# Optimization experiments

Measured on AMD Instinct MI355X. Metric: run time of the kernel, lower is better.

## Reference

```python
import jax, jax.numpy as jnp
import numpy as np

B, T, D, K = 16, 4096, 256, 1024

def setup_inputs() -> dict:
    key = jax.random.key(0)
    k1, k2 = jax.random.split(key)
    inputs = jax.random.normal(k1, (B, T, D), dtype=jnp.float32)
    codebook = jax.random.normal(k2, (K, D), dtype=jnp.float32)
    return {"inputs": inputs, "codebook": codebook}

def reference(inputs, codebook):
    # argmin over squared distance == argmin over L2 distance (cdist p=2).
    x2 = jnp.sum(inputs * inputs, axis=-1, keepdims=True)          # [B,T,1]
    c2 = jnp.sum(codebook * codebook, axis=-1)                      # [K]
    xc = jnp.einsum('btd,kd->btk', inputs, codebook)                # [B,T,K]
    d2 = x2 + c2[None, None, :] - 2.0 * xc                          # [B,T,K]
    assignment = jnp.argmin(d2, axis=-1)                            # [B,T]
    quantized = codebook[assignment]                                # [B,T,D]
    # Straight-through estimator
    out = jax.lax.stop_gradient(quantized - inputs) + inputs
    return out
```

## Files before the change

kernel.cpp:

```cpp
#include <hip/hip_runtime.h>
#include <float.h>


typedef _Float16 f16;
typedef f16 f16x8 __attribute__((ext_vector_type(8)));
typedef f16 f16x4 __attribute__((ext_vector_type(4)));
typedef float f32x4 __attribute__((ext_vector_type(4)));

#define DDIM    256
#define KCODES  1024
#define NTOK    65536
#define TOKB    64
#define SMARGIN 0.1f

__global__ __launch_bounds__(256) void vq_prep(const float* __restrict__ cb,
                                               f16* __restrict__ cht,
                                               float* __restrict__ c2,
                                               unsigned* __restrict__ count) {
    const int k    = blockIdx.x * 4 + (threadIdx.x >> 6);
    const int lane = threadIdx.x & 63;
    const float4 v = *(const float4*)(cb + (size_t)k * DDIM + 4 * lane);
    f16x4 h; h[0] = (f16)v.x; h[1] = (f16)v.y; h[2] = (f16)v.z; h[3] = (f16)v.w;
    const int ct = k >> 4, m = k & 15;
    const int e  = 4 * lane;
    const int kt = e >> 5;
    const int s  = (e & 31) >> 3;
    const int j0 = e & 7;
    const int L  = s * 16 + m;
    *(f16x4*)(cht + ((size_t)(ct * 8 + kt) * 64 + L) * 8 + j0) = h;
    float ssum = v.x * v.x + v.y * v.y + v.z * v.z + v.w * v.w;
    #pragma unroll
    for (int off = 32; off > 0; off >>= 1) ssum += __shfl_down(ssum, off, 64);
    if (lane == 0) c2[k] = ssum;
    if (blockIdx.x == 0 && threadIdx.x == 0) *count = 0u;
}

#define SLICE(CUR, S, NPTR, NS) do {                                                \
    _Pragma("unroll")                                                               \
    for (int ci = 0; ci < 4; ++ci)                                                  \
        _Pragma("unroll")                                                           \
        for (int ti = 0; ti < 2; ++ti)                                              \
            acc[ci][ti] = __builtin_amdgcn_mfma_f32_16x16x32_f16(                   \
                CUR[ci], bfrag[ti][S], acc[ci][ti], 0, 0, 0);                       \
    _Pragma("unroll")                                                               \
    for (int ci = 0; ci < 4; ++ci)                                                  \
        CUR[ci] = *(const f16x8*)((NPTR) + ci * 4096 + (NS) * 512);                 \
} while (0)

__global__ __launch_bounds__(256, 3) void vq_main(const float* __restrict__ xg,
                                                  const f16* __restrict__ cht,
                                                  const float* __restrict__ c2,
                                                  const float* __restrict__ cb,
                                                  float* __restrict__ out,
                                                  unsigned* __restrict__ count,
                                                  unsigned* __restrict__ list) {
    __shared__ float c2s[KCODES];
    __shared__ float wmv[2][TOKB];
    __shared__ int   wmi[2][TOKB];
    __shared__ float wms[2][TOKB];
    __shared__ int   idx_s[TOKB];

    const int t    = threadIdx.x;
    const int wave = t >> 6, lane = t & 63;
    const int wm   = wave >> 1;
    const int tn   = wave & 1;
    const int q    = lane >> 4;
    const int m16  = lane & 15;
    const int tok0 = blockIdx.x * TOKB;

    *(float4*)&c2s[t * 4] = *(const float4*)(c2 + t * 4);
    __syncthreads();

    const f16* aw = cht + wm * 16384 + lane * 8;

    f16x8 afA[4], afB[4];
    #pragma unroll
    for (int ci = 0; ci < 4; ++ci) afA[ci] = *(const f16x8*)(aw + ci * 4096 + 0 * 512);
    #pragma unroll
    for (int ci = 0; ci < 4; ++ci) afB[ci] = *(const f16x8*)(aw + ci * 4096 + 1 * 512);

    f16x8 bfrag[2][8];
    #pragma unroll
    for (int ti = 0; ti < 2; ++ti) {
        const size_t row = (size_t)(tok0 + tn * 32 + ti * 16 + m16) * DDIM;
        #pragma unroll
        for (int ks = 0; ks < 8; ++ks) {
            const float* p = xg + row + ks * 32 + q * 8;
            const float4 u0 = *(const float4*)(p);
            const float4 u1 = *(const float4*)(p + 4);
            f16x8 b;
            b[0] = (f16)u0.x; b[1] = (f16)u0.y; b[2] = (f16)u0.z; b[3] = (f16)u0.w;
            b[4] = (f16)u1.x; b[5] = (f16)u1.y; b[6] = (f16)u1.z; b[7] = (f16)u1.w;
            bfrag[ti][ks] = b;
        }
    }

    float rb1[2], rb2[2];
    #pragma unroll
    for (int ti = 0; ti < 2; ++ti) { rb1[ti] = -FLT_MAX; rb2[ti] = -FLT_MAX; }

    #pragma unroll 1
    for (int nc = 0; nc < 8; ++nc) {
        f32x4 acc[4][2];
        #pragma unroll
        for (int ci = 0; ci < 4; ++ci) {
            f32x4 cv = *(const f32x4*)&c2s[nc * 128 + wm * 64 + ci * 16 + q * 4];
            cv = cv * -0.5f;
            #pragma unroll
            for (int ti = 0; ti < 2; ++ti) acc[ci][ti] = cv;
        }

        const f16* an = aw + nc * 32768;
        const f16* ax = aw + ((nc + 1) & 7) * 32768;

        __builtin_amdgcn_s_setprio(1);
        SLICE(afA, 0, an, 2);
        SLICE(afB, 1, an, 3);
        SLICE(afA, 2, an, 4);
        SLICE(afB, 3, an, 5);
        SLICE(afA, 4, an, 6);
        SLICE(afB, 5, an, 7);
        SLICE(afA, 6, ax, 0);
        SLICE(afB, 7, ax, 1);
        __builtin_amdgcn_s_setprio(0);

        #pragma unroll
        for (int ti = 0; ti < 2; ++ti) {
            #pragma unroll
            for (int ci = 0; ci < 4; ++ci) {
                #pragma unroll
                for (int r = 0; r < 4; ++r) {
                    const unsigned pv = (__float_as_uint(acc[ci][ti][r]) & ~127u)
                                        | (unsigned)(127 - (nc * 16 + ci * 4 + r));
                    const float pf = __uint_as_float(pv);
                    rb2[ti] = fmaxf(rb2[ti], fminf(rb1[ti], pf));
                    rb1[ti] = fmaxf(rb1[ti], pf);
                }
            }
        }
    }

    #pragma unroll
    for (int ti = 0; ti < 2; ++ti) {
        const int jj = 127 - (int)(__float_as_uint(rb1[ti]) & 127u);
        int   i1 = (jj >> 4) * 128 + wm * 64 + ((jj >> 2) & 3) * 16 + q * 4 + (jj & 3);
        float b1 = rb1[ti], b2 = rb2[ti];
        #pragma unroll
        for (int sft = 0; sft < 2; ++sft) {
            const int off = 16 << sft;
            const float ob1 = __shfl_xor(b1, off, 64);
            const float ob2 = __shfl_xor(b2, off, 64);
            const int   oi1 = __shfl_xor(i1, off, 64);
            const bool better = (ob1 > b1) || (ob1 == b1 && oi1 < i1);
            b2 = fmaxf(fmaxf(b2, ob2), fminf(b1, ob1));
            b1 = better ? ob1 : b1;
            i1 = better ? oi1 : i1;
        }
        if (lane < 16) {
            const int tl = tn * 32 + ti * 16 + m16;
            wmv[wm][tl] = b1; wmi[wm][tl] = i1; wms[wm][tl] = b2;
        }
    }
    __syncthreads();

    if (t < TOKB) {
        const float a1 = wmv[0][t], a2 = wms[0][t];
        const int   ai = wmi[0][t];
        const float b1_ = wmv[1][t], b2_ = wms[1][t];
        const int   bi_ = wmi[1][t];
        const bool bb = (b1_ > a1) || (b1_ == a1 && bi_ < ai);
        const float c1 = bb ? b1_ : a1;
        const int   ci_ = bb ? bi_ : ai;
        const float cs = fmaxf(fmaxf(a2, b2_), fminf(a1, b1_));
        idx_s[t] = ci_;
        if (c1 - cs < SMARGIN) {
            const unsigned p = atomicAdd(count, 1u);
            list[p] = tok0 + t;
        }
    }
    __syncthreads();

    #pragma unroll
    for (int i = 0; i < 16; ++i) {
        const int f   = i * 256 + t;
        const int tok = f >> 6, d4 = f & 63;
        const int code = idx_s[tok];
        const float4 v = *(const float4*)(cb + (size_t)code * DDIM + 4 * d4);
        *(float4*)(out + (size_t)(tok0 + tok) * DDIM + 4 * d4) = v;
    }
}

__global__ __launch_bounds__(256) void vq_rescue(const float* __restrict__ xg,
                                                 const float* __restrict__ cb,
                                                 const float* __restrict__ c2,
                                                 const unsigned* __restrict__ count,
                                                 const unsigned* __restrict__ list,
                                                 float* __restrict__ out) {
    __shared__ float xls[8][DDIM];
    __shared__ float rv[4][8];
    __shared__ int   ri[4][8];
    __shared__ int   bidx[8];

    const int t = threadIdx.x;
    const int wave = t >> 6, lane = t & 63;
    const unsigned n = *count;

    for (unsigned base = blockIdx.x * 8; base < n; base += gridDim.x * 8) {
        const int nb = (int)min(8u, n - base);
        __syncthreads();
        #pragma unroll
        for (int i = 0; i < 2; ++i) {
            const int f = t + 256 * i;
            const int row = f >> 6, d4 = f & 63;
            if (row < nb)
                *(float4*)&xls[row][4 * d4] =
                    *(const float4*)(xg + (size_t)list[base + row] * DDIM + 4 * d4);
        }
        __syncthreads();

        float acc[4][8];
        #pragma unroll
        for (int j = 0; j < 4; ++j)
            #pragma unroll
            for (int tk = 0; tk < 8; ++tk) acc[j][tk] = 0.0f;

        for (int d4 = 0; d4 < 64; ++d4) {
            float4 cv[4];
            #pragma unroll
            for (int j = 0; j < 4; ++j)
                cv[j] = *(const float4*)(cb + (size_t)(4 * t + j) * DDIM + 4 * d4);
            #pragma unroll
            for (int tk = 0; tk < 8; ++tk) {
                const float4 xv = *(const float4*)&xls[tk][4 * d4];
                #pragma unroll
                for (int j = 0; j < 4; ++j) {
                    float a = acc[j][tk];
                    a = fmaf(cv[j].x, xv.x, a);
                    a = fmaf(cv[j].y, xv.y, a);
                    a = fmaf(cv[j].z, xv.z, a);
                    a = fmaf(cv[j].w, xv.w, a);
                    acc[j][tk] = a;
                }
            }
        }

        #pragma unroll
        for (int tk = 0; tk < 8; ++tk) {
            if (tk < nb) {
                float b1 = FLT_MAX; int i1 = 0;
                #pragma unroll
                for (int j = 0; j < 4; ++j) {
                    const float d = fmaf(-2.0f, acc[j][tk], c2[4 * t + j]);
                    if (d < b1) { b1 = d; i1 = 4 * t + j; }
                }
                #pragma unroll
                for (int off = 32; off > 0; off >>= 1) {
                    const float ov = __shfl_xor(b1, off, 64);
                    const int   oi = __shfl_xor(i1, off, 64);
                    if (ov < b1 || (ov == b1 && oi < i1)) { b1 = ov; i1 = oi; }
                }
                if (lane == 0) { rv[wave][tk] = b1; ri[wave][tk] = i1; }
            }
        }
        __syncthreads();
        if (t < 8 && t < nb) {
            float bv = rv[0][t]; int bi = ri[0][t];
            #pragma unroll
            for (int w = 1; w < 4; ++w)
                if (rv[w][t] < bv || (rv[w][t] == bv && ri[w][t] < bi)) {
                    bv = rv[w][t]; bi = ri[w][t];
                }
            bidx[t] = bi;
        }
        __syncthreads();

        #pragma unroll
        for (int i = 0; i < 2; ++i) {
            const int f = t + 256 * i;
            const int row = f >> 6, d4 = f & 63;
            if (row < nb) {
                const int code = bidx[row];
                const float4 v = *(const float4*)(cb + (size_t)code * DDIM + 4 * d4);
                *(float4*)(out + (size_t)list[base + row] * DDIM + 4 * d4) = v;
            }
        }
    }
}

extern "C" void kernel_launch(void* const* d_in, const int* in_sizes, int n_in,
                              void* d_out, int out_size, void* d_ws, size_t ws_size,
                              hipStream_t stream) {
    const float* x  = (const float*)d_in[0];
    const float* cb = (const float*)d_in[1];
    float* out = (float*)d_out;

    char* ws = (char*)d_ws;
    f16*      cht   = (f16*)ws;
    float*    c2    = (float*)(ws + 524288);
    unsigned* count = (unsigned*)(ws + 528448);
    unsigned* list  = (unsigned*)(ws + 528512);

    hipLaunchKernelGGL(vq_prep,   dim3(KCODES / 4), dim3(256), 0, stream, cb, cht, c2, count);
    hipLaunchKernelGGL(vq_main,   dim3(NTOK / TOKB), dim3(256), 0, stream,
                       x, cht, c2, cb, out, count, list);
    hipLaunchKernelGGL(vq_rescue, dim3(1024),       dim3(256), 0, stream,
                       x, cb, c2, count, list, out);
}
```

Before: 240.7 us.

## Stage token tile in LDS and split codebook across all four waves

Each block now converts its 64-token input tile to f16 once, stores it in shared memory in MFMA layout, and every wave covers all 64 tokens. Work is split over waves by codebook slice (4 x 64 codes per chunk) instead of a 2x2 token/code split. Each codebook fragment loaded from global memory now feeds 4 token tiles instead of 2, halving codebook traffic per token. In exchange B fragments are reloaded from LDS every slice, LDS use grows by 32KB, and the accumulator register footprint doubles, which may hurt occupancy at the 3-blocks-per-CU bound.

Result: slower. 282.4 us (+17.3%).

```diff
diff --git a/kernel.cpp b/kernel.cpp
--- a/kernel.cpp
+++ b/kernel.cpp
@@ -35,16 +35,19 @@
     if (blockIdx.x == 0 && threadIdx.x == 0) *count = 0u;
 }
 
-#define SLICE(CUR, S, NPTR, NS) do {                                                \
+#define SLICE(AF, BF, S, NAP, NBS) do {                                             \
     _Pragma("unroll")                                                               \
     for (int ci = 0; ci < 4; ++ci)                                                  \
         _Pragma("unroll")                                                           \
-        for (int ti = 0; ti < 2; ++ti)                                              \
+        for (int ti = 0; ti < 4; ++ti)                                              \
             acc[ci][ti] = __builtin_amdgcn_mfma_f32_16x16x32_f16(                   \
-                CUR[ci], bfrag[ti][S], acc[ci][ti], 0, 0, 0);                       \
+                AF[ci], BF[ti], acc[ci][ti], 0, 0, 0);                              \
     _Pragma("unroll")                                                               \
     for (int ci = 0; ci < 4; ++ci)                                                  \
-        CUR[ci] = *(const f16x8*)((NPTR) + ci * 4096 + (NS) * 512);                 \
+        AF[ci] = *(const f16x8*)((NAP) + ci * 4096 + (NBS) * 512);                  \
+    _Pragma("unroll")                                                               \
+    for (int ti = 0; ti < 4; ++ti)                                                  \
+        BF[ti] = *(const f16x8*)(bls + ((ti * 8 + (NBS)) * 64 + lane) * 8);         \
 } while (0)
 
 __global__ __launch_bounds__(256, 3) void vq_main(const float* __restrict__ xg,
@@ -54,78 +57,81 @@
                                                   float* __restrict__ out,
                                                   unsigned* __restrict__ count,
                                                   unsigned* __restrict__ list) {
+    __shared__ f16   bls[TOKB * DDIM];
     __shared__ float c2s[KCODES];
-    __shared__ float wmv[2][TOKB];
-    __shared__ int   wmi[2][TOKB];
-    __shared__ float wms[2][TOKB];
+    __shared__ float wmv[4][TOKB];
+    __shared__ float wms[4][TOKB];
+    __shared__ int   wmi[4][TOKB];
     __shared__ int   idx_s[TOKB];
 
     const int t    = threadIdx.x;
     const int wave = t >> 6, lane = t & 63;
-    const int wm   = wave >> 1;
-    const int tn   = wave & 1;
     const int q    = lane >> 4;
     const int m16  = lane & 15;
     const int tok0 = blockIdx.x * TOKB;
 
+    {
+        const int rr = t >> 2;
+        const int ti_ = rr >> 4, m = rr & 15;
+        const float* xrow = xg + (size_t)(tok0 + rr) * DDIM;
+        #pragma unroll
+        for (int p = 0; p < 16; ++p) {
+            const int e  = (t & 3) * 64 + p * 4;
+            const float4 v = *(const float4*)(xrow + e);
+            f16x4 h; h[0] = (f16)v.x; h[1] = (f16)v.y; h[2] = (f16)v.z; h[3] = (f16)v.w;
+            const int kt = e >> 5;
+            const int s  = (e & 31) >> 3;
+            const int j0 = e & 7;
+            const int L  = s * 16 + m;
+            *(f16x4*)(bls + ((ti_ * 8 + kt) * 64 + L) * 8 + j0) = h;
+        }
+    }
     *(float4*)&c2s[t * 4] = *(const float4*)(c2 + t * 4);
     __syncthreads();
 
-    const f16* aw = cht + wm * 16384 + lane * 8;
-
-    f16x8 afA[4], afB[4];
+    const f16* aw = cht + wave * 16384 + lane * 8;
+
+    f16x8 afA[4], afB[4], bfA[4], bfB[4];
     #pragma unroll
     for (int ci = 0; ci < 4; ++ci) afA[ci] = *(const f16x8*)(aw + ci * 4096 + 0 * 512);
     #pragma unroll
     for (int ci = 0; ci < 4; ++ci) afB[ci] = *(const f16x8*)(aw + ci * 4096 + 1 * 512);
-
-    f16x8 bfrag[2][8];
-    #pragma unroll
-    for (int ti = 0; ti < 2; ++ti) {
-        const size_t row = (size_t)(tok0 + tn * 32 + ti * 16 + m16) * DDIM;
-        #pragma unroll
-        for (int ks = 0; ks < 8; ++ks) {
-            const float* p = xg + row + ks * 32 + q * 8;
-            const float4 u0 = *(const float4*)(p);
-            const float4 u1 = *(const float4*)(p + 4);
-            f16x8 b;
-            b[0] = (f16)u0.x; b[1] = (f16)u0.y; b[2] = (f16)u0.z; b[3] = (f16)u0.w;
-            b[4] = (f16)u1.x; b[5] = (f16)u1.y; b[6] = (f16)u1.z; b[7] = (f16)u1.w;
-            bfrag[ti][ks] = b;
-        }
-    }
-
-    float rb1[2], rb2[2];
-    #pragma unroll
-    for (int ti = 0; ti < 2; ++ti) { rb1[ti] = -FLT_MAX; rb2[ti] = -FLT_MAX; }
+    #pragma unroll
+    for (int ti = 0; ti < 4; ++ti) bfA[ti] = *(const f16x8*)(bls + ((ti * 8 + 0) * 64 + lane) * 8);
+    #pragma unroll
+    for (int ti = 0; ti < 4; ++ti) bfB[ti] = *(const f16x8*)(bls + ((ti * 8 + 1) * 64 + lane) * 8);
+
+    float rb1[4], rb2[4];
+    #pragma unroll
+    for (int ti = 0; ti < 4; ++ti) { rb1[ti] = -FLT_MAX; rb2[ti] = -FLT_MAX; }
 
     #pragma unroll 1
-    for (int nc = 0; nc < 8; ++nc) {
-        f32x4 acc[4][2];
+    for (int nc = 0; nc < 4; ++nc) {
+        f32x4 acc[4][4];
         #pragma unroll
         for (int ci = 0; ci < 4; ++ci) {
-            f32x4 cv = *(const f32x4*)&c2s[nc * 128 + wm * 64 + ci * 16 + q * 4];
+            f32x4 cv = *(const f32x4*)&c2s[nc * 256 + wave * 64 + ci * 16 + q * 4];
             cv = cv * -0.5f;
             #pragma unroll
-            for (int ti = 0; ti < 2; ++ti) acc[ci][ti] = cv;
-        }
-
-        const f16* an = aw + nc * 32768;
-        const f16* ax = aw + ((nc + 1) & 7) * 32768;
+            for (int ti = 0; ti < 4; ++ti) acc[ci][ti] = cv;
+        }
+
+        const f16* an = aw + nc * 65536;
+        const f16* ax = aw + ((nc + 1) & 3) * 65536;
 
         __builtin_amdgcn_s_setprio(1);
-        SLICE(afA, 0, an, 2);
-        SLICE(afB, 1, an, 3);
-        SLICE(afA, 2, an, 4);
-        SLICE(afB, 3, an, 5);
-        SLICE(afA, 4, an, 6);
-        SLICE(afB, 5, an, 7);
-        SLICE(afA, 6, ax, 0);
-        SLICE(afB, 7, ax, 1);
+        SLICE(afA, bfA, 0, an, 2);
+        SLICE(afB, bfB, 1, an, 3);
+        SLICE(afA, bfA, 2, an, 4);
+        SLICE(afB, bfB, 3, an, 5);
+        SLICE(afA, bfA, 4, an, 6);
+        SLICE(afB, bfB, 5, an, 7);
+        SLICE(afA, bfA, 6, ax, 0);
+        SLICE(afB, bfB, 7, ax, 1);
         __builtin_amdgcn_s_setprio(0);
 
         #pragma unroll
-        for (int ti = 0; ti < 2; ++ti) {
+        for (int ti = 0; ti < 4; ++ti) {
             #pragma unroll
             for (int ci = 0; ci < 4; ++ci) {
                 #pragma unroll
@@ -141,9 +147,9 @@
     }
 
     #pragma unroll
-    for (int ti = 0; ti < 2; ++ti) {
+    for (int ti = 0; ti < 4; ++ti) {
         const int jj = 127 - (int)(__float_as_uint(rb1[ti]) & 127u);
-        int   i1 = (jj >> 4) * 128 + wm * 64 + ((jj >> 2) & 3) * 16 + q * 4 + (jj & 3);
+        int   i1 = (jj >> 4) * 256 + wave * 64 + ((jj >> 2) & 3) * 16 + q * 4 + (jj & 3);
         float b1 = rb1[ti], b2 = rb2[ti];
         #pragma unroll
         for (int sft = 0; sft < 2; ++sft) {
@@ -157,21 +163,23 @@
             i1 = better ? oi1 : i1;
         }
         if (lane < 16) {
-            const int tl = tn * 32 + ti * 16 + m16;
-            wmv[wm][tl] = b1; wmi[wm][tl] = i1; wms[wm][tl] = b2;
+            const int tl = ti * 16 + m16;
+            wmv[wave][tl] = b1; wmi[wave][tl] = i1; wms[wave][tl] = b2;
         }
     }
     __syncthreads();
 
     if (t < TOKB) {
-        const float a1 = wmv[0][t], a2 = wms[0][t];
-        const int   ai = wmi[0][t];
-        const float b1_ = wmv[1][t], b2_ = wms[1][t];
-        const int   bi_ = wmi[1][t];
-        const bool bb = (b1_ > a1) || (b1_ == a1 && bi_ < ai);
-        const float c1 = bb ? b1_ : a1;
-        const int   ci_ = bb ? bi_ : ai;
-        const float cs = fmaxf(fmaxf(a2, b2_), fminf(a1, b1_));
+        float c1 = wmv[0][t], cs = wms[0][t];
+        int   ci_ = wmi[0][t];
+        #pragma unroll
+        for (int w = 1; w < 4; ++w) {
+            const float b1 = wmv[w][t], b2 = wms[w][t];
+            const int   bi = wmi[w][t];
+            const bool bb = (b1 > c1) || (b1 == c1 && bi < ci_);
+            cs = fmaxf(fmaxf(cs, b2), fminf(c1, b1));
+            if (bb) { c1 = b1; ci_ = bi; }
+        }
         idx_s[t] = ci_;
         if (c1 - cs < SMARGIN) {
             const unsigned p = atomicAdd(count, 1u);
```

## Double token tile per block and stage input fragments in LDS

Applied to the files above, without the earlier changes.

The token tile per block grows from 64 to 128, so each codebook fragment read from global/L2 feeds twice as many MFMAs. Input tokens are converted to fp16 once into a shared-memory buffer laid out in MFMA fragment order, and the B fragments are streamed from LDS per k-slice instead of being held in registers. The A-fragment pipeline deepens to four register buffers. In exchange, occupancy drops to 2 blocks per CU, LDS use rises by 64KB per block, and the grid is halved, which may leave CUs underfilled.

Result: faster. 218.2 us (-9.3%).

```diff
diff --git a/kernel.cpp b/kernel.cpp
--- a/kernel.cpp
+++ b/kernel.cpp
@@ -10,7 +10,7 @@
 #define DDIM    256
 #define KCODES  1024
 #define NTOK    65536
-#define TOKB    64
+#define TOKB    128
 #define SMARGIN 0.1f
 
 __global__ __launch_bounds__(256) void vq_prep(const float* __restrict__ cb,
@@ -35,29 +35,33 @@
     if (blockIdx.x == 0 && threadIdx.x == 0) *count = 0u;
 }
 
-#define SLICE(CUR, S, NPTR, NS) do {                                                \
+#define SLICE(AF, BF, S, AP, NSA, NSB) do {                                         \
     _Pragma("unroll")                                                               \
     for (int ci = 0; ci < 4; ++ci)                                                  \
         _Pragma("unroll")                                                           \
-        for (int ti = 0; ti < 2; ++ti)                                              \
+        for (int ti = 0; ti < 4; ++ti)                                              \
             acc[ci][ti] = __builtin_amdgcn_mfma_f32_16x16x32_f16(                   \
-                CUR[ci], bfrag[ti][S], acc[ci][ti], 0, 0, 0);                       \
+                AF[ci], BF[ti], acc[ci][ti], 0, 0, 0);                              \
     _Pragma("unroll")                                                               \
     for (int ci = 0; ci < 4; ++ci)                                                  \
-        CUR[ci] = *(const f16x8*)((NPTR) + ci * 4096 + (NS) * 512);                 \
+        AF[ci] = *(const f16x8*)((AP) + ci * 4096 + (NSA) * 512);                   \
+    _Pragma("unroll")                                                               \
+    for (int ti = 0; ti < 4; ++ti)                                                  \
+        BF[ti] = *(const f16x8*)(&bls[tnoff + ((ti * 8 + (NSB)) * 64 + lane) * 8]); \
 } while (0)
 
-__global__ __launch_bounds__(256, 3) void vq_main(const float* __restrict__ xg,
+__global__ __launch_bounds__(256, 2) void vq_main(const float* __restrict__ xg,
                                                   const f16* __restrict__ cht,
                                                   const float* __restrict__ c2,
                                                   const float* __restrict__ cb,
                                                   float* __restrict__ out,
                                                   unsigned* __restrict__ count,
                                                   unsigned* __restrict__ list) {
+    __shared__ f16   bls[TOKB * DDIM];
     __shared__ float c2s[KCODES];
     __shared__ float wmv[2][TOKB];
+    __shared__ float wms[2][TOKB];
     __shared__ int   wmi[2][TOKB];
-    __shared__ float wms[2][TOKB];
     __shared__ int   idx_s[TOKB];
 
     const int t    = threadIdx.x;
@@ -67,65 +71,71 @@
     const int q    = lane >> 4;
     const int m16  = lane & 15;
     const int tok0 = blockIdx.x * TOKB;
-
+    const int tnoff = tn * 16384;
+
+    #pragma unroll
+    for (int i = 0; i < 32; ++i) {
+        const int g  = i * 1024 + t * 4;
+        const int rr = g >> 8;
+        const int e  = g & 255;
+        const float4 v = *(const float4*)(xg + (size_t)(tok0 + rr) * DDIM + e);
+        f16x4 h; h[0] = (f16)v.x; h[1] = (f16)v.y; h[2] = (f16)v.z; h[3] = (f16)v.w;
+        const int kt  = e >> 5;
+        const int s   = (e & 31) >> 3;
+        const int j0  = e & 7;
+        const int ti_ = rr >> 4, m = rr & 15;
+        *(f16x4*)(&bls[((ti_ * 8 + kt) * 64 + s * 16 + m) * 8 + j0]) = h;
+    }
     *(float4*)&c2s[t * 4] = *(const float4*)(c2 + t * 4);
     __syncthreads();
 
     const f16* aw = cht + wm * 16384 + lane * 8;
 
-    f16x8 afA[4], afB[4];
-    #pragma unroll
-    for (int ci = 0; ci < 4; ++ci) afA[ci] = *(const f16x8*)(aw + ci * 4096 + 0 * 512);
-    #pragma unroll
-    for (int ci = 0; ci < 4; ++ci) afB[ci] = *(const f16x8*)(aw + ci * 4096 + 1 * 512);
-
-    f16x8 bfrag[2][8];
-    #pragma unroll
-    for (int ti = 0; ti < 2; ++ti) {
-        const size_t row = (size_t)(tok0 + tn * 32 + ti * 16 + m16) * DDIM;
-        #pragma unroll
-        for (int ks = 0; ks < 8; ++ks) {
-            const float* p = xg + row + ks * 32 + q * 8;
-            const float4 u0 = *(const float4*)(p);
-            const float4 u1 = *(const float4*)(p + 4);
-            f16x8 b;
-            b[0] = (f16)u0.x; b[1] = (f16)u0.y; b[2] = (f16)u0.z; b[3] = (f16)u0.w;
-            b[4] = (f16)u1.x; b[5] = (f16)u1.y; b[6] = (f16)u1.z; b[7] = (f16)u1.w;
-            bfrag[ti][ks] = b;
-        }
-    }
-
-    float rb1[2], rb2[2];
-    #pragma unroll
-    for (int ti = 0; ti < 2; ++ti) { rb1[ti] = -FLT_MAX; rb2[ti] = -FLT_MAX; }
+    f16x8 afA[4], afB[4], afC[4], afD[4], bfA[4], bfB[4];
+    #pragma unroll
+    for (int ci = 0; ci < 4; ++ci) {
+        afA[ci] = *(const f16x8*)(aw + ci * 4096 + 0 * 512);
+        afB[ci] = *(const f16x8*)(aw + ci * 4096 + 1 * 512);
+        afC[ci] = *(const f16x8*)(aw + ci * 4096 + 2 * 512);
+        afD[ci] = *(const f16x8*)(aw + ci * 4096 + 3 * 512);
+    }
+    #pragma unroll
+    for (int ti = 0; ti < 4; ++ti) {
+        bfA[ti] = *(const f16x8*)(&bls[tnoff + ((ti * 8 + 0) * 64 + lane) * 8]);
+        bfB[ti] = *(const f16x8*)(&bls[tnoff + ((ti * 8 + 1) * 64 + lane) * 8]);
+    }
+
+    float rb1[4], rb2[4];
+    #pragma unroll
+    for (int ti = 0; ti < 4; ++ti) { rb1[ti] = -FLT_MAX; rb2[ti] = -FLT_MAX; }
 
     #pragma unroll 1
     for (int nc = 0; nc < 8; ++nc) {
-        f32x4 acc[4][2];
+        f32x4 acc[4][4];
         #pragma unroll
         for (int ci = 0; ci < 4; ++ci) {
             f32x4 cv = *(const f32x4*)&c2s[nc * 128 + wm * 64 + ci * 16 + q * 4];
             cv = cv * -0.5f;
             #pragma unroll
-            for (int ti = 0; ti < 2; ++ti) acc[ci][ti] = cv;
+            for (int ti = 0; ti < 4; ++ti) acc[ci][ti] = cv;
         }
 
         const f16* an = aw + nc * 32768;
         const f16* ax = aw + ((nc + 1) & 7) * 32768;
 
         __builtin_amdgcn_s_setprio(1);
-        SLICE(afA, 0, an, 2);
-        SLICE(afB, 1, an, 3);
-        SLICE(afA, 2, an, 4);
-        SLICE(afB, 3, an, 5);
-        SLICE(afA, 4, an, 6);
-        SLICE(afB, 5, an, 7);
-        SLICE(afA, 6, ax, 0);
-        SLICE(afB, 7, ax, 1);
+        SLICE(afA, bfA, 0, an, 4, 2);
+        SLICE(afB, bfB, 1, an, 5, 3);
+        SLICE(afC, bfA, 2, an, 6, 4);
+        SLICE(afD, bfB, 3, an, 7, 5);
+        SLICE(afA, bfA, 4, ax, 0, 6);
+        SLICE(afB, bfB, 5, ax, 1, 7);
+        SLICE(afC, bfA, 6, ax, 2, 0);
+        SLICE(afD, bfB, 7, ax, 3, 1);
         __builtin_amdgcn_s_setprio(0);
 
         #pragma unroll
-        for (int ti = 0; ti < 2; ++ti) {
+        for (int ti = 0; ti < 4; ++ti) {
             #pragma unroll
             for (int ci = 0; ci < 4; ++ci) {
                 #pragma unroll
@@ -141,7 +151,7 @@
     }
 
     #pragma unroll
-    for (int ti = 0; ti < 2; ++ti) {
+    for (int ti = 0; ti < 4; ++ti) {
         const int jj = 127 - (int)(__float_as_uint(rb1[ti]) & 127u);
         int   i1 = (jj >> 4) * 128 + wm * 64 + ((jj >> 2) & 3) * 16 + q * 4 + (jj & 3);
         float b1 = rb1[ti], b2 = rb2[ti];
@@ -157,7 +167,7 @@
             i1 = better ? oi1 : i1;
         }
         if (lane < 16) {
-            const int tl = tn * 32 + ti * 16 + m16;
+            const int tl = tn * 64 + ti * 16 + m16;
             wmv[wm][tl] = b1; wmi[wm][tl] = i1; wms[wm][tl] = b2;
         }
     }
@@ -181,7 +191,7 @@
     __syncthreads();
 
     #pragma unroll
-    for (int i = 0; i < 16; ++i) {
+    for (int i = 0; i < 32; ++i) {
         const int f   = i * 256 + t;
         const int tok = f >> 6, d4 = f & 63;
         const int code = idx_s[tok];
```
